# Optimization experiments

Measured on AMD Instinct MI355X. Metric: run time of the kernel, lower is better.

## Reference

```python
import jax, jax.numpy as jnp
import numpy as np
from jax import lax

# dims (see shape_source)
B, C, H, W = 2, 128, 48, 48
HEADS = 4
G = 4                 # offset_groups = heads
DH = C // HEADS       # 32, dim_head
DF = 4                # downsample_factor
OKS = 6               # offset_kernel_size
PAD = (OKS - DF) // 2 # 1
OFFSET_SCALE = 4.0
CPB_DIM = C // 4      # 32
OD = C // G           # offset_dims = 32


def setup_inputs() -> dict:
    key = jax.random.key(0)
    ks = jax.random.split(key, 12)
    rn = lambda k, shape, s=0.05: jax.random.normal(k, shape, dtype=jnp.float32) * s
    return {
        "x": jax.random.normal(ks[0], (B, C, H, W), dtype=jnp.float32),
        "gamma": jax.random.normal(ks[1], (1,), dtype=jnp.float32),  # nn.Parameter([0.0]); randomized so both paths contribute
        "wq": rn(ks[2], (G, DH, C // G)),    # grouped 1x1 conv, groups=G
        "wk": rn(ks[3], (G, DH, C // G)),
        "wv": rn(ks[4], (G, DH, C // G)),
        "wo": rn(ks[5], (C, C)),             # to_out 1x1 conv
        "bo": jnp.zeros((C,), jnp.float32),
        "w_off_dw": rn(ks[6], (OD, 1, OKS, OKS)),  # depthwise conv k=6 s=4 p=1
        "b_off_dw": jnp.zeros((OD,), jnp.float32),
        "w_off_proj": rn(ks[7], (2, OD)),          # 1x1 conv to 2 offset channels, no bias
        "cpb_w0": rn(ks[8], (2, CPB_DIM), 0.5),
        "cpb_b0": jnp.zeros((CPB_DIM,), jnp.float32),
        "cpb_w1": rn(ks[9], (CPB_DIM, CPB_DIM), 0.2),
        "cpb_b1": jnp.zeros((CPB_DIM,), jnp.float32),
        "cpb_w2": rn(ks[10], (CPB_DIM, HEADS // G), 0.2),
        "cpb_b2": jnp.zeros((HEADS // G,), jnp.float32),
    }


def _bilinear_sample(img, px, py):
    """F.grid_sample(mode='bilinear', padding_mode='zeros') on pixel coords.
    img: (N, Cg, Hi, Wi); px, py: (N, Ho, Wo) -> (N, Cg, Ho, Wo)"""
    N, Cg, Hi, Wi = img.shape
    imgf = img.reshape(N, Cg, Hi * Wi)
    x0 = jnp.floor(px)
    y0 = jnp.floor(py)
    wx1 = px - x0
    wy1 = py - y0

    def corner(xc, yc, w):
        valid = (xc >= 0) & (xc <= Wi - 1) & (yc >= 0) & (yc <= Hi - 1)
        xi = jnp.clip(xc, 0, Wi - 1).astype(jnp.int32)
        yi = jnp.clip(yc, 0, Hi - 1).astype(jnp.int32)
        idx = (yi * Wi + xi).reshape(N, -1)
        vals = jnp.take_along_axis(imgf, idx[:, None, :], axis=2)  # (N,Cg,Ho*Wo)
        return vals * (w * valid).reshape(N, 1, -1)

    out = (corner(x0, y0, (1 - wx1) * (1 - wy1))
           + corner(x0 + 1, y0, wx1 * (1 - wy1))
           + corner(x0, y0 + 1, (1 - wx1) * wy1)
           + corner(x0 + 1, y0 + 1, wx1 * wy1))
    return out.reshape(N, Cg, px.shape[1], px.shape[2])


def _forward(x, gamma, wq, wk, wv, wo, bo, w_off_dw, b_off_dw, w_off_proj,
             cpb_w0, cpb_b0, cpb_w1, cpb_b1, cpb_w2, cpb_b2):
    b = x.shape[0]
    scale = DH ** -0.5
    xg = x.reshape(b, G, C // G, H, W)
    # grouped 1x1 conv -> queries (b, G, DH, H, W); channel layout (g d) == (h d) since G==HEADS
    q = jnp.einsum('bgchw,goc->bgohw', xg, wq)
    gq = q.reshape(b * G, DH, H, W)
    # to_offsets: depthwise conv (k=6, s=4, p=1) -> GELU -> 1x1 to 2ch -> tanh -> *offset_scale
    off = lax.conv_general_dilated(gq, w_off_dw, (DF, DF), [(PAD, PAD), (PAD, PAD)],
                                   feature_group_count=OD,
                                   dimension_numbers=('NCHW', 'OIHW', 'NCHW'))
    off = jax.nn.gelu(off + b_off_dw[None, :, None, None], approximate=False)
    off = jnp.tanh(jnp.einsum('bchw,oc->bohw', off, w_off_proj)) * OFFSET_SCALE  # (bG,2,Hd,Wd)
    Hd, Wd = off.shape[-2], off.shape[-1]
    gy, gx = jnp.meshgrid(jnp.arange(Hd, dtype=jnp.float32),
                          jnp.arange(Wd, dtype=jnp.float32), indexing='ij')
    vg0 = gx[None] + off[:, 0]  # channel 0 = x (meshgrid 'xy' in torch code)
    vg1 = gy[None] + off[:, 1]  # channel 1 = y
    vn0 = 2.0 * vg0 / max(Hd - 1, 1) - 1.0  # normalize_grid (H==W so h/w quirk is moot)
    vn1 = 2.0 * vg1 / max(Wd - 1, 1) - 1.0
    # grid_sample align_corners=False unnormalization: pix = ((u+1)*size - 1)/2
    px = ((vn0 + 1.0) * W - 1.0) / 2.0
    py = ((vn1 + 1.0) * H - 1.0) / 2.0
    kv = _bilinear_sample(xg.reshape(b * G, C // G, H, W), px, py)  # (bG, C/G, Hd, Wd)
    kvg = kv.reshape(b, G, C // G, Hd, Wd)
    k = jnp.einsum('bgchw,goc->bgohw', kvg, wk)
    v = jnp.einsum('bgchw,goc->bgohw', kvg, wv)
    i, j = H * W, Hd * Wd
    qh = q.reshape(b, HEADS, DH, i).transpose(0, 1, 3, 2) * scale  # (b,h,i,d)
    kh = k.reshape(b, HEADS, DH, j).transpose(0, 1, 3, 2)
    vh = v.reshape(b, HEADS, DH, j).transpose(0, 1, 3, 2)
    sim = jnp.einsum('bhid,bhjd->bhij', qh, kh)
    # CPB relative position bias
    gyq, gxq = jnp.meshgrid(jnp.arange(H, dtype=jnp.float32),
                            jnp.arange(W, dtype=jnp.float32), indexing='ij')
    qn0 = 2.0 * gxq / max(H - 1, 1) - 1.0
    qn1 = 2.0 * gyq / max(W - 1, 1) - 1.0
    grid_q = jnp.stack([qn0, qn1], -1).reshape(1, i, 1, 2)
    grid_kv = jnp.stack([vn0, vn1], -1).reshape(b * G, 1, j, 2)
    pos = grid_q - grid_kv                       # (bG, i, j, 2)
    bias = jnp.sign(pos) * jnp.log1p(jnp.abs(pos))
    h1 = jax.nn.relu(bias @ cpb_w0 + cpb_b0)
    h2 = jax.nn.relu(h1 @ cpb_w1 + cpb_b1)
    bias = h2 @ cpb_w2 + cpb_b2                  # (bG, i, j, heads//G)
    bias = bias.reshape(b, G, i, j, HEADS // G).transpose(0, 1, 4, 2, 3).reshape(b, HEADS, i, j)
    attn = jax.nn.softmax(sim + bias, axis=-1)
    outh = jnp.einsum('bhij,bhjd->bhid', attn, vh)
    out = outh.transpose(0, 1, 3, 2).reshape(b, C, H, W)  # 'b h (x y) d -> b (h d) x y'
    attention = jnp.einsum('bchw,oc->bohw', out, wo) + bo[None, :, None, None]
    return gamma[0] * attention + x, attention


def reference(x, gamma, wq, wk, wv, wo, bo, w_off_dw, b_off_dw, w_off_proj,
              cpb_w0, cpb_b0, cpb_w1, cpb_b1, cpb_w2, cpb_b2):
    return _forward(x, gamma, wq, wk, wv, wo, bo, w_off_dw, b_off_dw, w_off_proj,
                    cpb_w0, cpb_b0, cpb_w1, cpb_b1, cpb_w2, cpb_b2)
```

## Files before the change

### kernel.cpp

```cpp
#include <hip/hip_runtime.h>
#include <math.h>

#define HWHW 2304
#define JD   144
#define LSP  148

typedef __attribute__((ext_vector_type(8))) short short8;
typedef __attribute__((ext_vector_type(4))) float f32x4;
typedef __attribute__((ext_vector_type(2))) float f32x2;

__device__ inline ushort f2bf(float f) {
  uint u = __float_as_uint(f);
  u += 0x7fffu + ((u >> 16) & 1u);
  return (ushort)(u >> 16);
}
__device__ inline float bf2f(ushort s) { return __uint_as_float((uint)s << 16); }
__device__ inline uint packbf(float hi, float lo) {
  return __builtin_amdgcn_perm(__float_as_uint(hi), __float_as_uint(lo), 0x07060302);
}


__global__ __launch_bounds__(384) void offset_kv_kernel(
    const float* __restrict__ x, const float* __restrict__ wq,
    const float* __restrict__ wdw, const float* __restrict__ bdw,
    const float* __restrict__ wproj, const float* __restrict__ wk,
    const float* __restrict__ wv,
    float* __restrict__ vn0, float* __restrict__ vn1,
    ushort* __restrict__ ktb, ushort* __restrict__ vtb) {
  __shared__ float qs[288][33];
  __shared__ float wdws[36][32];
  __shared__ float wkl[32][33], wvl[32][33];
  __shared__ float kvs[32][13];
  __shared__ float spx[12], spy[12];
  int hd = blockIdx.x, bg = blockIdx.y, b = bg >> 2, g = bg & 3;
  int t = threadIdx.x;
  int w = t >> 6, lane = t & 63, lam = lane & 15, quad = lane >> 4;

  {
    int hy = hd * 4 - 1 + w;
    if (hy >= 0 && hy < 48) {
      const float* wqg = wq + (g * 32) * 32;
      float4 wa = *(const float4*)(wqg + lam * 32 + quad * 8);
      float4 wb = *(const float4*)(wqg + lam * 32 + quad * 8 + 4);
      float4 wc = *(const float4*)(wqg + (16 + lam) * 32 + quad * 8);
      float4 wd = *(const float4*)(wqg + (16 + lam) * 32 + quad * 8 + 4);
      union { uint u[4]; short8 s8; } bf0, bf1;
      bf0.u[0] = packbf(wa.y, wa.x); bf0.u[1] = packbf(wa.w, wa.z);
      bf0.u[2] = packbf(wb.y, wb.x); bf0.u[3] = packbf(wb.w, wb.z);
      bf1.u[0] = packbf(wc.y, wc.x); bf1.u[1] = packbf(wc.w, wc.z);
      bf1.u[2] = packbf(wd.y, wd.x); bf1.u[3] = packbf(wd.w, wd.z);
      const float* xg = x + (b * 128 + g * 32) * HWHW + hy * 48;
#pragma unroll
      for (int tt = 0; tt < 3; ++tt) {
        int col = tt * 16 + lam;
        union { uint u[4]; short8 s8; } xa;
#pragma unroll
        for (int j = 0; j < 4; ++j) {
          float x0 = xg[(quad * 8 + 2 * j) * HWHW + col];
          float x1 = xg[(quad * 8 + 2 * j + 1) * HWHW + col];
          xa.u[j] = packbf(x1, x0);
        }
        f32x4 z = {0.f, 0.f, 0.f, 0.f};
        f32x4 d0 = __builtin_amdgcn_mfma_f32_16x16x32_bf16(xa.s8, bf0.s8, z, 0, 0, 0);
        f32x4 d1 = __builtin_amdgcn_mfma_f32_16x16x32_bf16(xa.s8, bf1.s8, z, 0, 0, 0);
        int p = w * 48 + tt * 16 + quad * 4;
#pragma unroll
        for (int r = 0; r < 4; ++r) {
          qs[p + r][lam] = d0[r];
          qs[p + r][16 + lam] = d1[r];
        }
      }
    } else {
#pragma unroll
      for (int tt = 0; tt < 3; ++tt) {
        int p = w * 48 + tt * 16 + quad * 4;
#pragma unroll
        for (int r = 0; r < 4; ++r) {
          qs[p + r][lam] = 0.f;
          qs[p + r][16 + lam] = 0.f;
        }
      }
    }
  }
  for (int u = t; u < 1152; u += 384) wdws[u >> 5][u & 31] = wdw[(u & 31) * 36 + (u >> 5)];
  for (int u = t; u < 1024; u += 384) {
    int d = u >> 5, c = u & 31;
    wkl[d][c] = wk[g * 1024 + u];
    wvl[d][c] = wv[g * 1024 + u];
  }
  __syncthreads();
  {
    int wd = t >> 5, c = t & 31;
    float s = 0.f;
#pragma unroll
    for (int ky = 0; ky < 6; ++ky) {
#pragma unroll
      for (int kx = 0; kx < 6; ++kx) {
        int wx = wd * 4 - 1 + kx;
        if (wx >= 0 && wx < 48)
          s += wdws[ky * 6 + kx][c] * qs[ky * 48 + wx][c];
      }
    }
    s += bdw[c];
    s = 0.5f * s * (1.f + erff(s * 0.70710678118654752f));
    float g0 = wproj[c] * s;
    float g1 = wproj[32 + c] * s;
#pragma unroll
    for (int k = 16; k >= 1; k >>= 1) {
      g0 += __shfl_xor(g0, k, 64);
      g1 += __shfl_xor(g1, k, 64);
    }
    if (c == 0) {
      float off0 = tanhf(g0) * 4.f;
      float off1 = tanhf(g1) * 4.f;
      float n0 = 2.f * ((float)wd + off0) / 11.f - 1.f;
      float n1 = 2.f * ((float)hd + off1) / 11.f - 1.f;
      int idx = bg * JD + hd * 12 + wd;
      vn0[idx] = n0;
      vn1[idx] = n1;
      spx[wd] = ((n0 + 1.f) * 48.f - 1.f) * 0.5f;
      spy[wd] = ((n1 + 1.f) * 48.f - 1.f) * 0.5f;
    }
  }
  __syncthreads();
  {
    int j = t >> 5, c = t & 31;
    float fx = spx[j], fy = spy[j];
    float x0 = floorf(fx), y0 = floorf(fy);
    float wx = fx - x0, wy = fy - y0;
    int xi = (int)x0, yi = (int)y0;
    const float* xp = x + (b * 128 + g * 32 + c) * HWHW;
    float v00 = 0.f, v10 = 0.f, v01 = 0.f, v11 = 0.f;
    bool okx0 = (xi >= 0) & (xi < 48), okx1 = (xi + 1 >= 0) & (xi + 1 < 48);
    if (yi >= 0 && yi < 48) {
      if (okx0) v00 = xp[yi * 48 + xi];
      if (okx1) v10 = xp[yi * 48 + xi + 1];
    }
    if (yi + 1 >= 0 && yi + 1 < 48) {
      if (okx0) v01 = xp[(yi + 1) * 48 + xi];
      if (okx1) v11 = xp[(yi + 1) * 48 + xi + 1];
    }
    kvs[c][j] = v00 * (1.f - wx) * (1.f - wy) + v10 * wx * (1.f - wy)
              + v01 * (1.f - wx) * wy + v11 * wx * wy;
  }
  __syncthreads();
  {
    int j = t >> 5, d = t & 31;
    float ak = 0.f, av = 0.f;
#pragma unroll
    for (int c = 0; c < 32; ++c) {
      float val = kvs[c][j];
      ak += wkl[d][c] * val;
      av += wvl[d][c] * val;
    }
    int jg = hd * 12 + j;
    ktb[bg * 4608 + jg * 32 + d] = f2bf(ak);
    vtb[bg * 5120 + d * 160 + jg] = f2bf(av);
  }
  if (hd == 0) {
    for (int u = t; u < 512; u += 384)
      vtb[bg * 5120 + (u >> 4) * 160 + 144 + (u & 15)] = 0;
  }
}

__global__ __launch_bounds__(256) void attn_fused_kernel(
    const float* __restrict__ x, const float* __restrict__ wq,
    const ushort* __restrict__ ktb, const ushort* __restrict__ vtb,
    const float* __restrict__ vn0, const float* __restrict__ vn1,
    const float* __restrict__ w0, const float* __restrict__ b0,
    const float* __restrict__ w1, const float* __restrict__ b1,
    const float* __restrict__ w2, const float* __restrict__ b2,
    ushort* __restrict__ outh) {
  __shared__ __align__(16) char smem[30080];
  float* Ls = (float*)smem;
  f32x2* st = (f32x2*)(smem + 9472);
  ushort* qbf = (ushort*)(smem + 27904);
  float* sv0 = (float*)(smem + 28928);
  float* sv1 = (float*)(smem + 29504);

  int bg = blockIdx.y, b = bg >> 2, g = bg & 3;
  int i0 = blockIdx.x * 16;
  int t = threadIdx.x;
  int w = t >> 6, lane = t & 63;
  int lam = lane & 15, quad = lane >> 4;

  if (t < JD) { sv0[t] = vn0[bg * JD + t]; sv1[t] = vn1[bg * JD + t]; }

  {
    const float* wqg = wq + (g * 32) * 32;
    float4 wa = *(const float4*)(wqg + lam * 32 + quad * 8);
    float4 wb = *(const float4*)(wqg + lam * 32 + quad * 8 + 4);
    float4 wc = *(const float4*)(wqg + (16 + lam) * 32 + quad * 8);
    float4 wd = *(const float4*)(wqg + (16 + lam) * 32 + quad * 8 + 4);
    union { uint u[4]; short8 s8; } bf0, bf1, xa;
    bf0.u[0] = packbf(wa.y, wa.x); bf0.u[1] = packbf(wa.w, wa.z);
    bf0.u[2] = packbf(wb.y, wb.x); bf0.u[3] = packbf(wb.w, wb.z);
    bf1.u[0] = packbf(wc.y, wc.x); bf1.u[1] = packbf(wc.w, wc.z);
    bf1.u[2] = packbf(wd.y, wd.x); bf1.u[3] = packbf(wd.w, wd.z);
    const float* xg = x + (b * 128 + g * 32) * HWHW + i0;
#pragma unroll
    for (int j = 0; j < 4; ++j) {
      float x0 = xg[(quad * 8 + 2 * j) * HWHW + lam];
      float x1 = xg[(quad * 8 + 2 * j + 1) * HWHW + lam];
      xa.u[j] = packbf(x1, x0);
    }
    f32x4 z = {0.f, 0.f, 0.f, 0.f};
    f32x4 d0 = __builtin_amdgcn_mfma_f32_16x16x32_bf16(xa.s8, bf0.s8, z, 0, 0, 0);
    f32x4 d1 = __builtin_amdgcn_mfma_f32_16x16x32_bf16(xa.s8, bf1.s8, z, 0, 0, 0);
#pragma unroll
    for (int r = 0; r < 4; ++r) {
      qbf[(quad * 4 + r) * 32 + lam] = f2bf(d0[r]);
      qbf[(quad * 4 + r) * 32 + 16 + lam] = f2bf(d1[r]);
    }
  }

  f32x2 w00r2[4], w01r2[4], b0r2[4];
#pragma unroll
  for (int j = 0; j < 4; ++j) {
    int k = quad * 8 + 2 * j;
    w00r2[j] = (f32x2){w0[k], w0[k + 1]};
    w01r2[j] = (f32x2){w0[32 + k], w0[32 + k + 1]};
    b0r2[j]  = (f32x2){b0[k], b0[k + 1]};
  }
  short8 w1f0, w1f1;
#pragma unroll
  for (int j = 0; j < 8; ++j) {
    int k = quad * 8 + j;
    w1f0[j] = (short)f2bf(w1[k * 32 + lam]);
    w1f1[j] = (short)f2bf(w1[k * 32 + 16 + lam]);
  }
  f32x4 zA, zB;
  f32x2 w2A01, w2A23, w2B01, w2B23;
#pragma unroll
  for (int r = 0; r < 4; ++r) {
    zA[r] = b1[quad * 4 + r];
    zB[r] = b1[16 + quad * 4 + r];
  }
  w2A01 = (f32x2){w2[quad * 4], w2[quad * 4 + 1]};
  w2A23 = (f32x2){w2[quad * 4 + 2], w2[quad * 4 + 3]};
  w2B01 = (f32x2){w2[16 + quad * 4], w2[16 + quad * 4 + 1]};
  w2B23 = (f32x2){w2[16 + quad * 4 + 2], w2[16 + quad * 4 + 3]};
  float b2s = b2[0];

  short8 vf[5];
  if (w < 2) {
    const ushort* vb = vtb + bg * 5120 + (w * 16 + lam) * 160;
#pragma unroll
    for (int kb = 0; kb < 5; ++kb)
      vf[kb] = *(const short8*)(vb + kb * 32 + quad * 8);
  }

  __syncthreads();

  const float scale = 0.17677669529663687f;
  {
    short8 aq = *(const short8*)(qbf + lam * 32 + quad * 8);
    const ushort* kb = ktb + bg * 4608;
#pragma unroll 1
    for (int jt = w; jt < 9; jt += 4) {
      short8 bk = *(const short8*)(kb + (jt * 16 + lam) * 32 + quad * 8);
      f32x4 acc = {0.f, 0.f, 0.f, 0.f};
      acc = __builtin_amdgcn_mfma_f32_16x16x32_bf16(aq, bk, acc, 0, 0, 0);
#pragma unroll
      for (int r = 0; r < 4; ++r)
        Ls[(quad * 4 + r) * LSP + jt * 16 + lam] = acc[r] * scale;
    }
  }

  {
    int iy = i0 / 48;
    int ix0 = i0 - iy * 48;
    float qn1 = (float)iy * (2.f / 47.f) - 1.f;
#pragma unroll 1
    for (int u = t; u < 2304; u += 256) {
      int r = u / 144, jj = u - r * 144;
      float qn0 = (float)(ix0 + r) * (2.f / 47.f) - 1.f;
      float p0 = qn0 - sv0[jj];
      float p1 = qn1 - sv1[jj];
      st[u] = (f32x2){copysignf(__logf(1.f + fabsf(p0)), p0),
                      copysignf(__logf(1.f + fabsf(p1)), p1)};
    }
  }
  __syncthreads();

  const f32x2 zero2 = {0.f, 0.f};
  int pbase = w * 576;
#pragma unroll 1
  for (int s = 0; s < 9; ++s) {
    float bm[4];
#pragma unroll
    for (int mt = 0; mt < 4; ++mt) {
      f32x2 sv = st[pbase + s * 64 + mt * 16 + lam];
      f32x2 s0v = {sv[0], sv[0]}, s1v = {sv[1], sv[1]};
      union { uint u[4]; short8 s8; } cvt;
#pragma unroll
      for (int j = 0; j < 4; ++j) {
        f32x2 hv = __builtin_elementwise_max(
            __builtin_elementwise_fma(s0v, w00r2[j],
                __builtin_elementwise_fma(s1v, w01r2[j], b0r2[j])), zero2);
        cvt.u[j] = packbf(hv[1], hv[0]);
      }
      f32x4 dA = __builtin_amdgcn_mfma_f32_16x16x32_bf16(w1f0, cvt.s8, zA, 0, 0, 0);
      f32x4 dB = __builtin_amdgcn_mfma_f32_16x16x32_bf16(w1f1, cvt.s8, zB, 0, 0, 0);
      f32x2 a01 = __builtin_elementwise_max((f32x2){dA[0], dA[1]}, zero2);
      f32x2 a23 = __builtin_elementwise_max((f32x2){dA[2], dA[3]}, zero2);
      f32x2 c01 = __builtin_elementwise_max((f32x2){dB[0], dB[1]}, zero2);
      f32x2 c23 = __builtin_elementwise_max((f32x2){dB[2], dB[3]}, zero2);
      f32x2 av = __builtin_elementwise_fma(a01, w2A01,
                 __builtin_elementwise_fma(a23, w2A23,
                 __builtin_elementwise_fma(c01, w2B01,
                 __builtin_elementwise_fma(c23, w2B23, zero2))));
      float acc = av[0] + av[1];
      acc += __shfl_xor(acc, 16, 64);
      acc += __shfl_xor(acc, 32, 64);
      bm[mt] = acc;
    }
    int P = s * 64 + lane;
    int ii = P / 144, jj = P - ii * 144;
    float biasv = (quad == 0 ? bm[0] : quad == 1 ? bm[1] : quad == 2 ? bm[2] : bm[3]) + b2s;
    Ls[(w * 4 + ii) * LSP + jj] += biasv;
  }
  __syncthreads();

  {
    int row = w * 4 + quad;
    float* Lp = Ls + row * LSP;
    float lv[9];
#pragma unroll
    for (int k = 0; k < 9; ++k) lv[k] = Lp[lam + 16 * k];
    float m = lv[0];
#pragma unroll
    for (int k = 1; k < 9; ++k) m = fmaxf(m, lv[k]);
#pragma unroll
    for (int k = 8; k >= 1; k >>= 1) m = fmaxf(m, __shfl_xor(m, k, 64));
    float e[9], sum = 0.f;
#pragma unroll
    for (int k = 0; k < 9; ++k) { e[k] = __expf(lv[k] - m); sum += e[k]; }
#pragma unroll
    for (int k = 8; k >= 1; k >>= 1) sum += __shfl_xor(sum, k, 64);
    float inv = 1.f / sum;
    ushort* pb = (ushort*)(Lp + 64);
#pragma unroll
    for (int k = 0; k < 9; ++k) pb[lam + 16 * k] = f2bf(e[k] * inv);
    pb[144 + lam] = 0;
  }
  __syncthreads();

  if (w < 2) {
    f32x4 o = {0.f, 0.f, 0.f, 0.f};
    const ushort* pb = (const ushort*)(Ls + lam * LSP + 64);
#pragma unroll
    for (int kb = 0; kb < 5; ++kb) {
      short8 ap = *(const short8*)(pb + kb * 32 + quad * 8);
      o = __builtin_amdgcn_mfma_f32_16x16x32_bf16(ap, vf[kb], o, 0, 0, 0);
    }
#pragma unroll
    for (int r = 0; r < 4; ++r) {
      int ig = i0 + quad * 4 + r;
      outh[((long)b * HWHW + ig) * 128 + g * 32 + w * 16 + lam] = f2bf(o[r]);
    }
  }
}

__global__ __launch_bounds__(256) void out_kernel(
    const ushort* __restrict__ outh, const float* __restrict__ wo,
    const float* __restrict__ bo, const float* __restrict__ x,
    const float* __restrict__ gamma, float* __restrict__ out) {
  int b = blockIdx.y;
  int hw0 = blockIdx.x * 16;
  int oc0 = blockIdx.z * 64;
  int t = threadIdx.x;
  int w = t >> 6, lane = t & 63, lam = lane & 15, quad = lane >> 4;
  const ushort* abase = outh + ((long)b * HWHW + hw0 + lam) * 128 + quad * 8;
  const float* wb0 = wo + (oc0 + w * 16 + lam) * 128 + quad * 8;
  f32x4 acc0 = {0.f, 0.f, 0.f, 0.f};
#pragma unroll
  for (int ks = 0; ks < 4; ++ks) {
    short8 a = *(const short8*)(abase + ks * 32);
    float4 wa = *(const float4*)(wb0 + ks * 32);
    float4 wb = *(const float4*)(wb0 + ks * 32 + 4);
    union { uint u[4]; short8 s8; } p0;
    p0.u[0] = packbf(wa.y, wa.x); p0.u[1] = packbf(wa.w, wa.z);
    p0.u[2] = packbf(wb.y, wb.x); p0.u[3] = packbf(wb.w, wb.z);
    acc0 = __builtin_amdgcn_mfma_f32_16x16x32_bf16(a, p0.s8, acc0, 0, 0, 0);
  }
  float gm = gamma[0];
  float* out0 = out;
  float* out1 = out + 2 * 128 * HWHW;
  {
    int oc = oc0 + w * 16 + lam;
    float bv = bo[oc];
    long base = ((long)(b * 128 + oc)) * HWHW + hw0 + quad * 4;
    float4 xv = *(const float4*)(x + base);
    float4 a1, a0;
    a1.x = acc0[0] + bv; a1.y = acc0[1] + bv; a1.z = acc0[2] + bv; a1.w = acc0[3] + bv;
    a0.x = fmaf(gm, a1.x, xv.x); a0.y = fmaf(gm, a1.y, xv.y);
    a0.z = fmaf(gm, a1.z, xv.z); a0.w = fmaf(gm, a1.w, xv.w);
    *(float4*)(out1 + base) = a1;
    *(float4*)(out0 + base) = a0;
  }
}

extern "C" void kernel_launch(void* const* d_in, const int* in_sizes, int n_in,
                              void* d_out, int out_size, void* d_ws, size_t ws_size,
                              hipStream_t stream) {
  const float* x     = (const float*)d_in[0];
  const float* gamma = (const float*)d_in[1];
  const float* wq    = (const float*)d_in[2];
  const float* wk    = (const float*)d_in[3];
  const float* wv    = (const float*)d_in[4];
  const float* wo    = (const float*)d_in[5];
  const float* bo    = (const float*)d_in[6];
  const float* wdw   = (const float*)d_in[7];
  const float* bdw   = (const float*)d_in[8];
  const float* wproj = (const float*)d_in[9];
  const float* cw0   = (const float*)d_in[10];
  const float* cb0   = (const float*)d_in[11];
  const float* cw1   = (const float*)d_in[12];
  const float* cb1   = (const float*)d_in[13];
  const float* cw2   = (const float*)d_in[14];
  const float* cb2   = (const float*)d_in[15];
  char* wsb = (char*)d_ws;
  float* vn0  = (float*)wsb;
  float* vn1  = (float*)(wsb + 4608);
  ushort* ktb = (ushort*)(wsb + 9216);
  ushort* vtb = (ushort*)(wsb + 82944);
  ushort* outh = (ushort*)(wsb + 164864);
  float* out  = (float*)d_out;

  offset_kv_kernel<<<dim3(12, 8), 384, 0, stream>>>(x, wq, wdw, bdw, wproj, wk, wv,
                                                    vn0, vn1, ktb, vtb);
  attn_fused_kernel<<<dim3(144, 8), 256, 0, stream>>>(x, wq, ktb, vtb, vn0, vn1,
                                                      cw0, cb0, cw1, cb1, cw2, cb2, outh);
  out_kernel<<<dim3(144, 2, 2), 256, 0, stream>>>(outh, wo, bo, x, gamma, out);
}
```

Before: 129.5 us.

## Fuse output projection into attention kernel via last-block atomic counter

Removes the separate out_kernel launch. Each attention block bumps a per-(batch, row-tile) atomic counter after writing its head-group slice, and the fourth block to arrive runs the 1x1 output projection, bias and residual for that tile. The counters are zeroed in the first kernel. This saves one launch and the gap between kernels, at the cost of threadfence and atomic synchronisation and a serialized tail done by one block per tile.

```diff
diff --git a/kernel.cpp b/kernel.cpp
--- a/kernel.cpp
+++ b/kernel.cpp
@@ -26,7 +26,8 @@
     const float* __restrict__ wproj, const float* __restrict__ wk,
     const float* __restrict__ wv,
     float* __restrict__ vn0, float* __restrict__ vn1,
-    ushort* __restrict__ ktb, ushort* __restrict__ vtb) {
+    ushort* __restrict__ ktb, ushort* __restrict__ vtb,
+    int* __restrict__ cnt) {
   __shared__ float qs[288][33];
   __shared__ float wdws[36][32];
   __shared__ float wkl[32][33], wvl[32][33];
@@ -35,6 +36,8 @@
   int hd = blockIdx.x, bg = blockIdx.y, b = bg >> 2, g = bg & 3;
   int t = threadIdx.x;
   int w = t >> 6, lane = t & 63, lam = lane & 15, quad = lane >> 4;
+
+  if (t < 3) cnt[(bg * 12 + hd) * 3 + t] = 0;
 
   {
     int hy = hd * 4 - 1 + w;
@@ -170,13 +173,17 @@
     const float* __restrict__ w0, const float* __restrict__ b0,
     const float* __restrict__ w1, const float* __restrict__ b1,
     const float* __restrict__ w2, const float* __restrict__ b2,
-    ushort* __restrict__ outh) {
-  __shared__ __align__(16) char smem[30080];
+    ushort* __restrict__ outh,
+    const float* __restrict__ wo, const float* __restrict__ bo,
+    const float* __restrict__ gamma, float* __restrict__ out,
+    int* __restrict__ cnt) {
+  __shared__ __align__(16) char smem[30096];
   float* Ls = (float*)smem;
   f32x2* st = (f32x2*)(smem + 9472);
   ushort* qbf = (ushort*)(smem + 27904);
   float* sv0 = (float*)(smem + 28928);
   float* sv1 = (float*)(smem + 29504);
+  int* flag = (int*)(smem + 30080);
 
   int bg = blockIdx.y, b = bg >> 2, g = bg & 3;
   int i0 = blockIdx.x * 16;
@@ -360,44 +367,45 @@
       outh[((long)b * HWHW + ig) * 128 + g * 32 + w * 16 + lam] = f2bf(o[r]);
     }
   }
-}
-
-__global__ __launch_bounds__(256) void out_kernel(
-    const ushort* __restrict__ outh, const float* __restrict__ wo,
-    const float* __restrict__ bo, const float* __restrict__ x,
-    const float* __restrict__ gamma, float* __restrict__ out) {
-  int b = blockIdx.y;
-  int hw0 = blockIdx.x * 16;
-  int oc0 = blockIdx.z * 64;
-  int t = threadIdx.x;
-  int w = t >> 6, lane = t & 63, lam = lane & 15, quad = lane >> 4;
-  const ushort* abase = outh + ((long)b * HWHW + hw0 + lam) * 128 + quad * 8;
-  const float* wb0 = wo + (oc0 + w * 16 + lam) * 128 + quad * 8;
-  f32x4 acc0 = {0.f, 0.f, 0.f, 0.f};
-#pragma unroll
-  for (int ks = 0; ks < 4; ++ks) {
-    short8 a = *(const short8*)(abase + ks * 32);
-    float4 wa = *(const float4*)(wb0 + ks * 32);
-    float4 wb = *(const float4*)(wb0 + ks * 32 + 4);
-    union { uint u[4]; short8 s8; } p0;
-    p0.u[0] = packbf(wa.y, wa.x); p0.u[1] = packbf(wa.w, wa.z);
-    p0.u[2] = packbf(wb.y, wb.x); p0.u[3] = packbf(wb.w, wb.z);
-    acc0 = __builtin_amdgcn_mfma_f32_16x16x32_bf16(a, p0.s8, acc0, 0, 0, 0);
-  }
-  float gm = gamma[0];
-  float* out0 = out;
-  float* out1 = out + 2 * 128 * HWHW;
-  {
-    int oc = oc0 + w * 16 + lam;
-    float bv = bo[oc];
-    long base = ((long)(b * 128 + oc)) * HWHW + hw0 + quad * 4;
-    float4 xv = *(const float4*)(x + base);
-    float4 a1, a0;
-    a1.x = acc0[0] + bv; a1.y = acc0[1] + bv; a1.z = acc0[2] + bv; a1.w = acc0[3] + bv;
-    a0.x = fmaf(gm, a1.x, xv.x); a0.y = fmaf(gm, a1.y, xv.y);
-    a0.z = fmaf(gm, a1.z, xv.z); a0.w = fmaf(gm, a1.w, xv.w);
-    *(float4*)(out1 + base) = a1;
-    *(float4*)(out0 + base) = a0;
+
+  __syncthreads();
+  if (t == 0) {
+    __threadfence();
+    int old = atomicAdd(cnt + b * 144 + blockIdx.x, 1);
+    if (old == 3) __threadfence();
+    *flag = (old == 3) ? 1 : 0;
+  }
+  __syncthreads();
+  if (*flag) {
+    const ushort* abase = outh + ((long)b * HWHW + i0 + lam) * 128 + quad * 8;
+    short8 af[4];
+#pragma unroll
+    for (int ks = 0; ks < 4; ++ks) af[ks] = *(const short8*)(abase + ks * 32);
+    float gm = gamma[0];
+#pragma unroll
+    for (int nt = 0; nt < 2; ++nt) {
+      int oc = w * 32 + nt * 16 + lam;
+      const float* wb0 = wo + oc * 128 + quad * 8;
+      f32x4 acc = {0.f, 0.f, 0.f, 0.f};
+#pragma unroll
+      for (int ks = 0; ks < 4; ++ks) {
+        float4 wa = *(const float4*)(wb0 + ks * 32);
+        float4 wb = *(const float4*)(wb0 + ks * 32 + 4);
+        union { uint u[4]; short8 s8; } p0;
+        p0.u[0] = packbf(wa.y, wa.x); p0.u[1] = packbf(wa.w, wa.z);
+        p0.u[2] = packbf(wb.y, wb.x); p0.u[3] = packbf(wb.w, wb.z);
+        acc = __builtin_amdgcn_mfma_f32_16x16x32_bf16(af[ks], p0.s8, acc, 0, 0, 0);
+      }
+      float bv = bo[oc];
+      long base = ((long)(b * 128 + oc)) * HWHW + i0 + quad * 4;
+      float4 xv = *(const float4*)(x + base);
+      float4 a1, a0;
+      a1.x = acc[0] + bv; a1.y = acc[1] + bv; a1.z = acc[2] + bv; a1.w = acc[3] + bv;
+      a0.x = fmaf(gm, a1.x, xv.x); a0.y = fmaf(gm, a1.y, xv.y);
+      a0.z = fmaf(gm, a1.z, xv.z); a0.w = fmaf(gm, a1.w, xv.w);
+      *(float4*)(out + 2 * 128 * HWHW + base) = a1;
+      *(float4*)(out + base) = a0;
+    }
   }
 }
 
@@ -426,11 +434,12 @@
   ushort* ktb = (ushort*)(wsb + 9216);
   ushort* vtb = (ushort*)(wsb + 82944);
   ushort* outh = (ushort*)(wsb + 164864);
+  int* cnt    = (int*)(wsb + 1344512);
   float* out  = (float*)d_out;
 
   offset_kv_kernel<<<dim3(12, 8), 384, 0, stream>>>(x, wq, wdw, bdw, wproj, wk, wv,
-                                                    vn0, vn1, ktb, vtb);
+                                                    vn0, vn1, ktb, vtb, cnt);
   attn_fused_kernel<<<dim3(144, 8), 256, 0, stream>>>(x, wq, ktb, vtb, vn0, vn1,
-                                                      cw0, cb0, cw1, cb1, cw2, cb2, outh);
-  out_kernel<<<dim3(144, 2, 2), 256, 0, stream>>>(outh, wo, bo, x, gamma, out);
+                                                      cw0, cb0, cw1, cb1, cw2, cb2, outh,
+                                                      wo, bo, gamma, out, cnt);
 }
```

Measured after the change: 158.7 us. 1.23x slower.

## Precompute separable log-position tables in offset kernel instead of per-block

Applied to the files above, without the earlier changes.

The signed-log relative position term separates by axis: the x-term depends only on the query column and key, the y-term only on the query row and key. The offset kernel now writes these two 48x144 tables per batch-group to workspace. The attention kernel loads them instead of evaluating 2304 pairs of logs per block, which also shrinks shared memory. The cost is extra global writes and reads, plus an integer divide in the inner bias loop to index the y-table.

```diff
diff --git a/kernel.cpp b/kernel.cpp
--- a/kernel.cpp
+++ b/kernel.cpp
@@ -25,13 +25,14 @@
     const float* __restrict__ wdw, const float* __restrict__ bdw,
     const float* __restrict__ wproj, const float* __restrict__ wk,
     const float* __restrict__ wv,
-    float* __restrict__ vn0, float* __restrict__ vn1,
-    ushort* __restrict__ ktb, ushort* __restrict__ vtb) {
+    ushort* __restrict__ ktb, ushort* __restrict__ vtb,
+    float* __restrict__ S0g, float* __restrict__ S1g) {
   __shared__ float qs[288][33];
   __shared__ float wdws[36][32];
   __shared__ float wkl[32][33], wvl[32][33];
   __shared__ float kvs[32][13];
   __shared__ float spx[12], spy[12];
+  __shared__ float spn0[12], spn1[12];
   int hd = blockIdx.x, bg = blockIdx.y, b = bg >> 2, g = bg & 3;
   int t = threadIdx.x;
   int w = t >> 6, lane = t & 63, lam = lane & 15, quad = lane >> 4;
@@ -115,9 +116,8 @@
       float off1 = tanhf(g1) * 4.f;
       float n0 = 2.f * ((float)wd + off0) / 11.f - 1.f;
       float n1 = 2.f * ((float)hd + off1) / 11.f - 1.f;
-      int idx = bg * JD + hd * 12 + wd;
-      vn0[idx] = n0;
-      vn1[idx] = n1;
+      spn0[wd] = n0;
+      spn1[wd] = n1;
       spx[wd] = ((n0 + 1.f) * 48.f - 1.f) * 0.5f;
       spy[wd] = ((n1 + 1.f) * 48.f - 1.f) * 0.5f;
     }
@@ -143,6 +143,21 @@
     kvs[c][j] = v00 * (1.f - wx) * (1.f - wy) + v10 * wx * (1.f - wy)
               + v01 * (1.f - wx) * wy + v11 * wx * wy;
   }
+  {
+#pragma unroll
+    for (int it = 0; it < 3; ++it) {
+      int u = t + it * 384;
+      int tab = u >= 576;
+      int idx = tab ? u - 576 : u;
+      int ii = idx / 12, wd = idx - ii * 12;
+      float qn = (float)ii * (2.f / 47.f) - 1.f;
+      float nv = tab ? spn1[wd] : spn0[wd];
+      float p = qn - nv;
+      float sres = copysignf(__logf(1.f + fabsf(p)), p);
+      float* dst = tab ? S1g : S0g;
+      dst[bg * 6912 + ii * 144 + hd * 12 + wd] = sres;
+    }
+  }
   __syncthreads();
   {
     int j = t >> 5, d = t & 31;
@@ -166,17 +181,16 @@
 __global__ __launch_bounds__(256) void attn_fused_kernel(
     const float* __restrict__ x, const float* __restrict__ wq,
     const ushort* __restrict__ ktb, const ushort* __restrict__ vtb,
-    const float* __restrict__ vn0, const float* __restrict__ vn1,
+    const float* __restrict__ S0g, const float* __restrict__ S1g,
     const float* __restrict__ w0, const float* __restrict__ b0,
     const float* __restrict__ w1, const float* __restrict__ b1,
     const float* __restrict__ w2, const float* __restrict__ b2,
     ushort* __restrict__ outh) {
-  __shared__ __align__(16) char smem[30080];
+  __shared__ __align__(16) char smem[20288];
   float* Ls = (float*)smem;
-  f32x2* st = (f32x2*)(smem + 9472);
-  ushort* qbf = (ushort*)(smem + 27904);
-  float* sv0 = (float*)(smem + 28928);
-  float* sv1 = (float*)(smem + 29504);
+  float* st0f = (float*)(smem + 9472);
+  float* st1f = (float*)(smem + 18688);
+  ushort* qbf = (ushort*)(smem + 19264);
 
   int bg = blockIdx.y, b = bg >> 2, g = bg & 3;
   int i0 = blockIdx.x * 16;
@@ -184,7 +198,14 @@
   int w = t >> 6, lane = t & 63;
   int lam = lane & 15, quad = lane >> 4;
 
-  if (t < JD) { sv0[t] = vn0[bg * JD + t]; sv1[t] = vn1[bg * JD + t]; }
+  {
+    int iy = i0 / 48;
+    int ix0 = i0 - iy * 48;
+    const float* S0p = S0g + bg * 6912 + ix0 * 144;
+#pragma unroll
+    for (int it = 0; it < 9; ++it) st0f[t + it * 256] = S0p[t + it * 256];
+    if (t < JD) st1f[t] = S1g[bg * 6912 + iy * 144 + t];
+  }
 
   {
     const float* wqg = wq + (g * 32) * 32;
@@ -266,21 +287,6 @@
         Ls[(quad * 4 + r) * LSP + jt * 16 + lam] = acc[r] * scale;
     }
   }
-
-  {
-    int iy = i0 / 48;
-    int ix0 = i0 - iy * 48;
-    float qn1 = (float)iy * (2.f / 47.f) - 1.f;
-#pragma unroll 1
-    for (int u = t; u < 2304; u += 256) {
-      int r = u / 144, jj = u - r * 144;
-      float qn0 = (float)(ix0 + r) * (2.f / 47.f) - 1.f;
-      float p0 = qn0 - sv0[jj];
-      float p1 = qn1 - sv1[jj];
-      st[u] = (f32x2){copysignf(__logf(1.f + fabsf(p0)), p0),
-                      copysignf(__logf(1.f + fabsf(p1)), p1)};
-    }
-  }
   __syncthreads();
 
   const f32x2 zero2 = {0.f, 0.f};
@@ -290,8 +296,11 @@
     float bm[4];
 #pragma unroll
     for (int mt = 0; mt < 4; ++mt) {
-      f32x2 sv = st[pbase + s * 64 + mt * 16 + lam];
-      f32x2 s0v = {sv[0], sv[0]}, s1v = {sv[1], sv[1]};
+      int Pm = pbase + s * 64 + mt * 16 + lam;
+      float s0 = st0f[Pm];
+      int iim = Pm / 144;
+      float s1 = st1f[Pm - iim * 144];
+      f32x2 s0v = {s0, s0}, s1v = {s1, s1};
       union { uint u[4]; short8 s8; } cvt;
 #pragma unroll
       for (int j = 0; j < 4; ++j) {
@@ -421,16 +430,16 @@
   const float* cw2   = (const float*)d_in[14];
   const float* cb2   = (const float*)d_in[15];
   char* wsb = (char*)d_ws;
-  float* vn0  = (float*)wsb;
-  float* vn1  = (float*)(wsb + 4608);
   ushort* ktb = (ushort*)(wsb + 9216);
   ushort* vtb = (ushort*)(wsb + 82944);
   ushort* outh = (ushort*)(wsb + 164864);
+  float* S0g  = (float*)(wsb + 1344512);
+  float* S1g  = (float*)(wsb + 1565696);
   float* out  = (float*)d_out;
 
   offset_kv_kernel<<<dim3(12, 8), 384, 0, stream>>>(x, wq, wdw, bdw, wproj, wk, wv,
-                                                    vn0, vn1, ktb, vtb);
-  attn_fused_kernel<<<dim3(144, 8), 256, 0, stream>>>(x, wq, ktb, vtb, vn0, vn1,
+                                                    ktb, vtb, S0g, S1g);
+  attn_fused_kernel<<<dim3(144, 8), 256, 0, stream>>>(x, wq, ktb, vtb, S0g, S1g,
                                                       cw0, cb0, cw1, cb1, cw2, cb2, outh);
   out_kernel<<<dim3(144, 2, 2), 256, 0, stream>>>(outh, wo, bo, x, gamma, out);
 }
```

Result: no change. 130.8 us (+1.0%).
